# Kernel optimization log

Hardware: AMD Instinct MI355X
Metric: run time of the kernel (lower is better)

Reference implementation:

```python
import jax, jax.numpy as jnp
import numpy as np
import math

B, L, D, H = 2, 2048, 1024, 16
DK = D // H

def setup_inputs() -> dict:
    key = jax.random.key(0)
    ks = jax.random.split(key, 12)
    s = 1.0 / math.sqrt(D)
    inp = {
        "Q": jax.random.normal(ks[0], (B, L, D), jnp.float32),
        "K": jax.random.normal(ks[1], (B, L, D), jnp.float32),
        "V": jax.random.normal(ks[2], (B, L, D), jnp.float32),
        "mask": jnp.tril(jnp.ones((L, L), jnp.bool_))[None, None],  # [1,1,L,L] causal
        "Wq_w": jax.random.normal(ks[3], (D, D), jnp.float32) * s,
        "Wq_b": jnp.zeros((D,), jnp.float32),
        "Wk_w": jax.random.normal(ks[4], (D, D), jnp.float32) * s,
        "Wk_b": jnp.zeros((D,), jnp.float32),
        "Wv_w": jax.random.normal(ks[5], (D, D), jnp.float32) * s,
        "Wv_b": jnp.zeros((D,), jnp.float32),
        "fc_w": jax.random.normal(ks[6], (D, D), jnp.float32) * s,
        "fc_b": jnp.zeros((D,), jnp.float32),
    }
    return inp

def reference(Q, K, V, mask, Wq_w, Wq_b, Wk_w, Wk_b, Wv_w, Wv_b, fc_w, fc_b):
    # torch Linear: y = x @ W.T + b
    def split_heads(x):
        return x.reshape(B, L, H, DK).transpose(0, 2, 1, 3)  # [B,H,L,DK]
    q = split_heads(Q @ Wq_w.T + Wq_b)
    k = split_heads(K @ Wk_w.T + Wk_b)
    v = split_heads(V @ Wv_w.T + Wv_b)
    scores = jnp.einsum("bhqd,bhkd->bhqk", q, k) / math.sqrt(DK)
    scores = jnp.where(mask, scores, jnp.float32(-1e9))
    attn = jax.nn.softmax(scores, axis=-1)
    out = jnp.einsum("bhqk,bhkd->bhqd", attn, v)
    out = out.transpose(0, 2, 1, 3).reshape(B, L, D)
    return out @ fc_w.T + fc_b
```

## Files before the change

### kernel.cpp

```cpp
#include <hip/hip_runtime.h>
#include <hip/hip_bf16.h>
#include <math.h>

typedef __attribute__((ext_vector_type(8))) short short8;
typedef __attribute__((ext_vector_type(4))) short short4v;
typedef __attribute__((ext_vector_type(4))) float float4v;
typedef __attribute__((ext_vector_type(2))) unsigned int uint2v;

static constexpr int Bc = 2, Lc = 2048, Dc = 1024, Hc = 16;
static constexpr float C1 = 0.125f * 1.44269504088896f;
static constexpr float C2 = -8.0f * 1.44269504088896f;

__device__ __forceinline__ short f2bf(float x) {
    unsigned int b = __float_as_uint(x);
    return (short)((b + 0x7FFFu + ((b >> 16) & 1u)) >> 16);
}

__device__ __forceinline__ void gld16(const void* g, void* l) {
    __builtin_amdgcn_global_load_lds(
        (const __attribute__((address_space(1))) unsigned int*)g,
        (__attribute__((address_space(3))) unsigned int*)l, 16, 0, 0);
}

__global__ __launch_bounds__(256) void cvt_all(
    const float* q, const float* k, const float* v,
    const float* wq, const float* wk, const float* wv, const float* fw,
    short* qo, short* ko, short* vo,
    short* wqo, short* wko, short* wvo, short* fwo)
{
    const int z = blockIdx.y;
    const float* s; short* d; int n;
    switch (z) {
        case 0: s = q;  d = qo;  n = Bc*Lc*Dc; break;
        case 1: s = k;  d = ko;  n = Bc*Lc*Dc; break;
        case 2: s = v;  d = vo;  n = Bc*Lc*Dc; break;
        case 3: s = wq; d = wqo; n = Dc*Dc; break;
        case 4: s = wk; d = wko; n = Dc*Dc; break;
        case 5: s = wv; d = wvo; n = Dc*Dc; break;
        default: s = fw; d = fwo; n = Dc*Dc; break;
    }
    const int idx = (blockIdx.x * 256 + threadIdx.x) * 8;
    if (idx >= n) return;
    float4 lo = *reinterpret_cast<const float4*>(s + idx);
    float4 hi = *reinterpret_cast<const float4*>(s + idx + 4);
    short8 o = short8{f2bf(lo.x), f2bf(lo.y), f2bf(lo.z), f2bf(lo.w),
                      f2bf(hi.x), f2bf(hi.y), f2bf(hi.z), f2bf(hi.w)};
    *reinterpret_cast<short8*>(d + idx) = o;
}

struct GemmCtx {
    int lane, w, wm, wn, quad, l16, bm0, bn0, srow, soct;
};
__device__ __forceinline__ void gemm_core(
    const short* __restrict__ A, const short* __restrict__ Bt,
    short* As, short* Bs, const GemmCtx& c, float4v acc[4][4])
{
    const int K = Dc;
    const int l7 = c.l16 & 7;
    for (int k0 = 0; k0 < K; k0 += 64) {
#pragma unroll
        for (int rep = 0; rep < 4; ++rep) {
            const int rb = (c.w * 4 + rep) * 8;
            const int goct = c.soct ^ c.srow;
            gld16(A  + (size_t)(c.bm0 + rb + c.srow) * K + k0 + goct * 8,
                  &As[rb * 64]);
            gld16(Bt + (size_t)(c.bn0 + rb + c.srow) * K + k0 + goct * 8,
                  &Bs[rb * 64]);
        }
        __syncthreads();
#pragma unroll
        for (int s = 0; s < 2; ++s) {
            const int roct = (s * 4 + c.quad) ^ l7;
            short8 af[4], bf[4];
#pragma unroll
            for (int i = 0; i < 4; ++i)
                af[i] = *reinterpret_cast<const short8*>(
                    &As[(c.wm * 64 + i * 16 + c.l16) * 64 + roct * 8]);
#pragma unroll
            for (int j = 0; j < 4; ++j)
                bf[j] = *reinterpret_cast<const short8*>(
                    &Bs[(c.wn * 64 + j * 16 + c.l16) * 64 + roct * 8]);
#pragma unroll
            for (int i = 0; i < 4; ++i)
#pragma unroll
                for (int j = 0; j < 4; ++j)
                    acc[i][j] = __builtin_amdgcn_mfma_f32_16x16x32_bf16(af[i], bf[j], acc[i][j], 0, 0, 0);
        }
        __syncthreads();
    }
}
__device__ __forceinline__ GemmCtx make_ctx() {
    GemmCtx c;
    const int tid = threadIdx.x;
    c.lane = tid & 63; c.w = tid >> 6;
    c.wm = c.w >> 1;   c.wn = c.w & 1;
    c.quad = c.lane >> 4; c.l16 = c.lane & 15;
    c.bm0 = blockIdx.y * 128; c.bn0 = blockIdx.x * 128;
    c.srow = c.lane >> 3; c.soct = c.lane & 7;
    return c;
}

__global__ __launch_bounds__(256, 2) void qkv_gemm(
    const short* __restrict__ Qb, const short* __restrict__ Kb, const short* __restrict__ Vb,
    const short* __restrict__ Wq, const short* __restrict__ Wk, const short* __restrict__ Wv,
    const float* __restrict__ bq, const float* __restrict__ bk, const float* __restrict__ bv,
    short* __restrict__ q_ws, short* __restrict__ k_ws, short* __restrict__ vT_ws)
{
    __shared__ short As[128 * 64];
    __shared__ short Bs[128 * 64];
    const int z = blockIdx.z;
    const short* A    = (z == 0) ? Qb : (z == 1) ? Kb : Vb;
    const short* Bt   = (z == 0) ? Wq : (z == 1) ? Wk : Wv;
    const float* bias = (z == 0) ? bq : (z == 1) ? bk : bv;

    GemmCtx c = make_ctx();
    float4v acc[4][4] = {};
    gemm_core(A, Bt, As, Bs, c, acc);

    if (z < 2) {
        short* C = (z == 0) ? q_ws : k_ws;
#pragma unroll
        for (int j = 0; j < 4; ++j) {
            const int col = c.bn0 + c.wn * 64 + j * 16 + c.l16;
            const float bv2 = bias[col];
#pragma unroll
            for (int i = 0; i < 4; ++i)
#pragma unroll
                for (int r = 0; r < 4; ++r) {
                    const int row = c.bm0 + c.wm * 64 + i * 16 + c.quad * 4 + r;
                    C[(size_t)row * Dc + col] = f2bf(acc[i][j][r] + bv2);
                }
        }
    } else {
#pragma unroll
        for (int j = 0; j < 4; ++j) {
            const int col = c.bn0 + c.wn * 64 + j * 16 + c.l16;
            const float bv2 = bias[col];
            const int hh = col >> 6, d = col & 63;
#pragma unroll
            for (int i = 0; i < 4; ++i) {
                const int row0 = c.bm0 + c.wm * 64 + i * 16 + c.quad * 4;
                const int bb = row0 >> 11, l = row0 & 2047;
                short4v o4;
#pragma unroll
                for (int r = 0; r < 4; ++r) o4[r] = f2bf(acc[i][j][r] + bv2);
                *reinterpret_cast<short4v*>(
                    &vT_ws[((size_t)((bb * 16 + hh) * 64 + d)) * Lc + l]) = o4;
            }
        }
    }
}

__global__ __launch_bounds__(256, 2) void out_gemm(
    const short* __restrict__ A, const short* __restrict__ Bt,
    const float* __restrict__ bias, float* __restrict__ C)
{
    __shared__ short As[128 * 64];
    __shared__ short Bs[128 * 64];
    GemmCtx c = make_ctx();
    float4v acc[4][4] = {};
    gemm_core(A, Bt, As, Bs, c, acc);
#pragma unroll
    for (int j = 0; j < 4; ++j) {
        const int col = c.bn0 + c.wn * 64 + j * 16 + c.l16;
        const float bv2 = bias[col];
#pragma unroll
        for (int i = 0; i < 4; ++i)
#pragma unroll
            for (int r = 0; r < 4; ++r) {
                const int row = c.bm0 + c.wm * 64 + i * 16 + c.quad * 4 + r;
                C[(size_t)row * Dc + col] = acc[i][j][r] + bv2;
            }
    }
}

__global__ __launch_bounds__(256, 4) void attn_flash7(
    const short* __restrict__ q_ws,
    const short* __restrict__ k_ws,
    const short* __restrict__ vT_ws,
    short* __restrict__ o_ws)
{
    __shared__ short Ks[2][64 * 64];
    __shared__ short Vs[2][64 * 64];

    const int tid  = threadIdx.x;
    const int lane = tid & 63;
    const int w    = tid >> 6;
    const int quad = lane >> 4;
    const int l16  = lane & 15;
    const int l7   = l16 & 7;

    const int id = blockIdx.x;
    const int g  = id >> 8;
    const int s  = (id >> 5) & 7;
    const int bh = id & 31;
    const int qi = (g == 0) ? (31 - s) : (g == 1) ? (23 - s)
                 : (g == 2) ? s        : (8 + s);
    const int b  = bh >> 4, h = bh & 15;

    const int srow = lane >> 3;
    const int soct = lane & 7;
    const size_t khead  = (size_t)(b * Lc) * Dc + h * 64;
    const size_t vthead = (size_t)(bh * 64) * Lc;
    const int xoct0 = quad ^ l7;
    const int xoct1 = (4 + quad) ^ l7;

    const short onev = (l16 == 0) ? (short)0x3F80 : (short)0;
    const short4v vb4 = short4v{onev, onev, onev, onev};

    auto stage = [&](int tile, int buf) {
#pragma unroll
        for (int rep = 0; rep < 2; ++rep) {
            const int issue = w * 2 + rep;
            const int grow = issue * 8 + srow;
            const int goct = soct ^ (grow & 7);
            gld16(k_ws + khead + (size_t)(tile * 64 + grow) * Dc + goct * 8,
                  &Ks[buf][issue * 512]);
            gld16(vT_ws + vthead + (size_t)grow * Lc + tile * 64 + goct * 8,
                  &Vs[buf][issue * 512]);
        }
    };

    const int q0   = qi * 64;
    const int qw0  = q0 + w * 16;
    const int qrow = qw0 + l16;

    short8 qf[2];
    {
        const size_t base = ((size_t)(b * Lc + qw0 + l16)) * Dc + h * 64;
        qf[0] = *reinterpret_cast<const short8*>(&q_ws[base + quad * 8]);
        qf[1] = *reinterpret_cast<const short8*>(&q_ws[base + 32 + quad * 8]);
    }

    float4v o_acc[5] = {};

    stage(0, 0);

#pragma unroll 1
    for (int kb = 0; kb <= qi; ++kb) {
        const int cur = kb & 1;
        if (kb < qi) {
            stage(kb + 1, cur ^ 1);
            asm volatile("s_waitcnt vmcnt(4)" ::: "memory");
        } else {
            asm volatile("s_waitcnt vmcnt(0)" ::: "memory");
        }
        __builtin_amdgcn_s_barrier();
        asm volatile("" ::: "memory");

        const short* Kc = &Ks[cur][0];
        const short* Vc = &Vs[cur][0];

        if (kb < qi) {
#pragma unroll
            for (int t = 0; t < 4; ++t) {
                short8 kf0 = *reinterpret_cast<const short8*>(&Kc[(t * 16 + l16) * 64 + xoct0 * 8]);
                short8 kf1 = *reinterpret_cast<const short8*>(&Kc[(t * 16 + l16) * 64 + xoct1 * 8]);
                float4v sv = {};
                sv = __builtin_amdgcn_mfma_f32_16x16x32_bf16(kf0, qf[0], sv, 0, 0, 0);
                sv = __builtin_amdgcn_mfma_f32_16x16x32_bf16(kf1, qf[1], sv, 0, 0, 0);

                short4v vb[4];
#pragma unroll
                for (int dt = 0; dt < 4; ++dt)
                    vb[dt] = *reinterpret_cast<const short4v*>(
                        &Vc[(dt * 16 + l16) * 64 + ((2 * t + (quad >> 1)) ^ l7) * 8 + (quad & 1) * 4]);

                unsigned u[4];
#pragma unroll
                for (int r = 0; r < 4; ++r)
                    u[r] = __float_as_uint(exp2f(fmaf(sv[r], C1, C2)));
                const uint2v pu = {(u[1] & 0xFFFF0000u) | (u[0] >> 16),
                                   (u[3] & 0xFFFF0000u) | (u[2] >> 16)};
                const short4v pa = __builtin_bit_cast(short4v, pu);

#pragma unroll
                for (int dt = 0; dt < 4; ++dt)
                    o_acc[dt] = __builtin_amdgcn_mfma_f32_16x16x16bf16_1k(pa, vb[dt], o_acc[dt], 0, 0, 0);
                o_acc[4] = __builtin_amdgcn_mfma_f32_16x16x16bf16_1k(pa, vb4, o_acc[4], 0, 0, 0);
            }
        } else {
#pragma unroll
            for (int t = 0; t < 4; ++t) {
                if (t <= w) {
                    short8 kf0 = *reinterpret_cast<const short8*>(&Kc[(t * 16 + l16) * 64 + xoct0 * 8]);
                    short8 kf1 = *reinterpret_cast<const short8*>(&Kc[(t * 16 + l16) * 64 + xoct1 * 8]);
                    float4v sv = {};
                    sv = __builtin_amdgcn_mfma_f32_16x16x32_bf16(kf0, qf[0], sv, 0, 0, 0);
                    sv = __builtin_amdgcn_mfma_f32_16x16x32_bf16(kf1, qf[1], sv, 0, 0, 0);

                    short4v vb[4];
#pragma unroll
                    for (int dt = 0; dt < 4; ++dt)
                        vb[dt] = *reinterpret_cast<const short4v*>(
                            &Vc[(dt * 16 + l16) * 64 + ((2 * t + (quad >> 1)) ^ l7) * 8 + (quad & 1) * 4]);

                    const int kbase = kb * 64 + t * 16 + quad * 4;
                    unsigned u[4];
                    if (t < w) {
#pragma unroll
                        for (int r = 0; r < 4; ++r)
                            u[r] = __float_as_uint(exp2f(fmaf(sv[r], C1, C2)));
                    } else {
#pragma unroll
                        for (int r = 0; r < 4; ++r) {
                            const float pv = (kbase + r <= qrow)
                                           ? exp2f(fmaf(sv[r], C1, C2)) : 0.f;
                            u[r] = __float_as_uint(pv);
                        }
                    }
                    const uint2v pu = {(u[1] & 0xFFFF0000u) | (u[0] >> 16),
                                       (u[3] & 0xFFFF0000u) | (u[2] >> 16)};
                    const short4v pa = __builtin_bit_cast(short4v, pu);

#pragma unroll
                    for (int dt = 0; dt < 4; ++dt)
                        o_acc[dt] = __builtin_amdgcn_mfma_f32_16x16x16bf16_1k(pa, vb[dt], o_acc[dt], 0, 0, 0);
                    o_acc[4] = __builtin_amdgcn_mfma_f32_16x16x16bf16_1k(pa, vb4, o_acc[4], 0, 0, 0);
                }
            }
        }
        asm volatile("" ::: "memory");
        __builtin_amdgcn_s_barrier();
    }

#pragma unroll
    for (int r = 0; r < 4; ++r) {
        const float lsum = __shfl(o_acc[4][r], quad << 4, 64);
        const float inv = 1.f / lsum;
        const int qr = qw0 + quad * 4 + r;
#pragma unroll
        for (int dt = 0; dt < 4; ++dt)
            o_ws[((size_t)(b * Lc + qr)) * Dc + h * 64 + dt * 16 + l16] =
                f2bf(o_acc[dt][r] * inv);
    }
}

extern "C" void kernel_launch(void* const* d_in, const int* in_sizes, int n_in,
                              void* d_out, int out_size, void* d_ws, size_t ws_size,
                              hipStream_t stream)
{
    const float* Q = (const float*)d_in[0];
    const float* K = (const float*)d_in[1];
    const float* V = (const float*)d_in[2];

    int w0 = -1;
    for (int i = 3; i + 8 <= n_in; ++i) {
        bool ok = true;
        for (int j = 0; j < 4 && ok; ++j)
            ok = (in_sizes[i + 2 * j] == Dc * Dc) && (in_sizes[i + 2 * j + 1] == Dc);
        if (ok) { w0 = i; break; }
    }
    if (w0 < 0) w0 = (n_in >= 12) ? 4 : 3;

    const float* Wq_w = (const float*)d_in[w0 + 0];
    const float* Wq_b = (const float*)d_in[w0 + 1];
    const float* Wk_w = (const float*)d_in[w0 + 2];
    const float* Wk_b = (const float*)d_in[w0 + 3];
    const float* Wv_w = (const float*)d_in[w0 + 4];
    const float* Wv_b = (const float*)d_in[w0 + 5];
    const float* fc_w = (const float*)d_in[w0 + 6];
    const float* fc_b = (const float*)d_in[w0 + 7];
    float* out = (float*)d_out;

    const size_t nel = (size_t)Bc * Lc * Dc;
    const size_t nw  = (size_t)Dc * Dc;
    short* p = (short*)d_ws;
    short* xq   = p;  p += nel;
    short* xk   = p;  p += nel;
    short* xv   = p;  p += nel;
    short* wqb  = p;  p += nw;
    short* wkb  = p;  p += nw;
    short* wvb  = p;  p += nw;
    short* fwb  = p;  p += nw;
    short* q_ws = p;  p += nel;
    short* k_ws = p;  p += nel;
    short* vT_ws= p;  p += nel;
    short* a_ws = xq;

    cvt_all<<<dim3(2048, 7), 256, 0, stream>>>(
        Q, K, V, Wq_w, Wk_w, Wv_w, fc_w, xq, xk, xv, wqb, wkb, wvb, fwb);

    qkv_gemm<<<dim3(8, 32, 3), 256, 0, stream>>>(
        xq, xk, xv, wqb, wkb, wvb, Wq_b, Wk_b, Wv_b, q_ws, k_ws, vT_ws);

    attn_flash7<<<dim3(1024), 256, 0, stream>>>(q_ws, k_ws, vT_ws, a_ws);

    out_gemm<<<dim3(8, 32), 256, 0, stream>>>(a_ws, fwb, fc_b, out);
}
```

Measured before the change: 226.4 us.

## Double-buffer GEMM LDS tiles and pack bf16 probabilities with v_perm

The shared GEMM core now uses two LDS buffers per operand and prefetches the next K tile with global_load_lds before computing on the current one. A partial vmcnt wait and barriers replace the per-iteration syncthreads pair, so global loads can overlap with the MFMA work. Separately, in the attention kernel the mask/shift/or that packs two bf16 values becomes a single v_perm byte permute. Doubling LDS to 64KB per block may lower occupancy below the two blocks per CU requested by the launch bounds.

```diff
diff --git a/kernel.cpp b/kernel.cpp
--- a/kernel.cpp
+++ b/kernel.cpp
@@ -53,21 +53,26 @@
 };
 __device__ __forceinline__ void gemm_core(
     const short* __restrict__ A, const short* __restrict__ Bt,
-    short* As, short* Bs, const GemmCtx& c, float4v acc[4][4])
+    short* As, short* Bs,
+    const GemmCtx& c, float4v acc[4][4])
 {
     const int K = Dc;
     const int l7 = c.l16 & 7;
-    for (int k0 = 0; k0 < K; k0 += 64) {
+    const int goct = c.soct ^ c.srow;
+
+    auto stage = [&](int k0, int buf) {
 #pragma unroll
         for (int rep = 0; rep < 4; ++rep) {
             const int rb = (c.w * 4 + rep) * 8;
-            const int goct = c.soct ^ c.srow;
             gld16(A  + (size_t)(c.bm0 + rb + c.srow) * K + k0 + goct * 8,
-                  &As[rb * 64]);
+                  &As[buf * 8192 + rb * 64]);
             gld16(Bt + (size_t)(c.bn0 + rb + c.srow) * K + k0 + goct * 8,
-                  &Bs[rb * 64]);
-        }
-        __syncthreads();
+                  &Bs[buf * 8192 + rb * 64]);
+        }
+    };
+    auto compute = [&](int buf) {
+        const short* Asb = &As[buf * 8192];
+        const short* Bsb = &Bs[buf * 8192];
 #pragma unroll
         for (int s = 0; s < 2; ++s) {
             const int roct = (s * 4 + c.quad) ^ l7;
@@ -75,19 +80,34 @@
 #pragma unroll
             for (int i = 0; i < 4; ++i)
                 af[i] = *reinterpret_cast<const short8*>(
-                    &As[(c.wm * 64 + i * 16 + c.l16) * 64 + roct * 8]);
+                    &Asb[(c.wm * 64 + i * 16 + c.l16) * 64 + roct * 8]);
 #pragma unroll
             for (int j = 0; j < 4; ++j)
                 bf[j] = *reinterpret_cast<const short8*>(
-                    &Bs[(c.wn * 64 + j * 16 + c.l16) * 64 + roct * 8]);
+                    &Bsb[(c.wn * 64 + j * 16 + c.l16) * 64 + roct * 8]);
 #pragma unroll
             for (int i = 0; i < 4; ++i)
 #pragma unroll
                 for (int j = 0; j < 4; ++j)
                     acc[i][j] = __builtin_amdgcn_mfma_f32_16x16x32_bf16(af[i], bf[j], acc[i][j], 0, 0, 0);
         }
-        __syncthreads();
-    }
+    };
+
+    stage(0, 0);
+#pragma unroll 1
+    for (int it = 0; it < 15; ++it) {
+        stage((it + 1) * 64, (it & 1) ^ 1);
+        asm volatile("s_waitcnt vmcnt(8)" ::: "memory");
+        __builtin_amdgcn_s_barrier();
+        asm volatile("" ::: "memory");
+        compute(it & 1);
+        asm volatile("" ::: "memory");
+        __builtin_amdgcn_s_barrier();
+    }
+    asm volatile("s_waitcnt vmcnt(0)" ::: "memory");
+    __builtin_amdgcn_s_barrier();
+    asm volatile("" ::: "memory");
+    compute(1);
 }
 __device__ __forceinline__ GemmCtx make_ctx() {
     GemmCtx c;
@@ -106,8 +126,8 @@
     const float* __restrict__ bq, const float* __restrict__ bk, const float* __restrict__ bv,
     short* __restrict__ q_ws, short* __restrict__ k_ws, short* __restrict__ vT_ws)
 {
-    __shared__ short As[128 * 64];
-    __shared__ short Bs[128 * 64];
+    __shared__ short As[2 * 128 * 64];
+    __shared__ short Bs[2 * 128 * 64];
     const int z = blockIdx.z;
     const short* A    = (z == 0) ? Qb : (z == 1) ? Kb : Vb;
     const short* Bt   = (z == 0) ? Wq : (z == 1) ? Wk : Wv;
@@ -155,8 +175,8 @@
     const short* __restrict__ A, const short* __restrict__ Bt,
     const float* __restrict__ bias, float* __restrict__ C)
 {
-    __shared__ short As[128 * 64];
-    __shared__ short Bs[128 * 64];
+    __shared__ short As[2 * 128 * 64];
+    __shared__ short Bs[2 * 128 * 64];
     GemmCtx c = make_ctx();
     float4v acc[4][4] = {};
     gemm_core(A, Bt, As, Bs, c, acc);
@@ -270,8 +290,8 @@
 #pragma unroll
                 for (int r = 0; r < 4; ++r)
                     u[r] = __float_as_uint(exp2f(fmaf(sv[r], C1, C2)));
-                const uint2v pu = {(u[1] & 0xFFFF0000u) | (u[0] >> 16),
-                                   (u[3] & 0xFFFF0000u) | (u[2] >> 16)};
+                const uint2v pu = {__builtin_amdgcn_perm(u[1], u[0], 0x07060302u),
+                                   __builtin_amdgcn_perm(u[3], u[2], 0x07060302u)};
                 const short4v pa = __builtin_bit_cast(short4v, pu);
 
 #pragma unroll
@@ -309,8 +329,8 @@
                             u[r] = __float_as_uint(pv);
                         }
                     }
-                    const uint2v pu = {(u[1] & 0xFFFF0000u) | (u[0] >> 16),
-                                       (u[3] & 0xFFFF0000u) | (u[2] >> 16)};
+                    const uint2v pu = {__builtin_amdgcn_perm(u[1], u[0], 0x07060302u),
+                                       __builtin_amdgcn_perm(u[3], u[2], 0x07060302u)};
                     const short4v pa = __builtin_bit_cast(short4v, pu);
 
 #pragma unroll
```

After: 230.7 us. Within noise of the previous version (+1.9%).
